# Optimization experiments

Hardware: AMD Instinct MI355X
Metric: run time of the kernel (lower is better)

Reference implementation:

```python
import jax, jax.numpy as jnp
import numpy as np

C = 1024        # number of classes
N = 8           # proxies per class
ALLNUM = C * N  # 8192 total proxies
DIM = 512
R = 0.05
TOPK = int(np.ceil(R * ALLNUM))  # 410
LAM = 0.3
B = 2048


def setup_inputs() -> dict:
    key = jax.random.key(0)
    k1, k2, k3 = jax.random.split(key, 3)
    inp = jax.random.normal(k1, (B, DIM), dtype=jnp.float32)
    target = jax.random.randint(k2, (B,), 0, C, dtype=jnp.int64)
    # kaiming-uniform-initialized proxies approximated by scaled normal init
    proxies = jax.random.normal(k3, (DIM, ALLNUM), dtype=jnp.float32)
    instance_label = jnp.repeat(jnp.arange(C, dtype=jnp.int64), N)  # [ALLNUM]
    return {"input": inp, "target": target, "Proxies": proxies,
            "instance_label": instance_label}


def reference(input, target, Proxies, instance_label):
    # L2-normalize each proxy column (F.normalize along dim=0, eps=1e-12)
    norm = jnp.maximum(jnp.linalg.norm(Proxies, axis=0, keepdims=True), 1e-12)
    centers = Proxies / norm                             # [DIM, ALLNUM]
    similarity = input @ centers                          # [B, ALLNUM]

    positive_mask = (target[:, None] == instance_label[None, :]).astype(similarity.dtype)
    _, indices = jax.lax.top_k(similarity + 1000.0 * positive_mask, TOPK)  # [B, TOPK]

    rows = jnp.arange(similarity.shape[0])[:, None]
    mask = jnp.zeros_like(similarity).at[rows, indices].set(1.0)
    prob_a = mask * similarity                            # sparse-masked similarities

    y_instance_onehot = jax.nn.one_hot(instance_label, C, dtype=similarity.dtype)  # [ALLNUM, C]
    logits = prob_a @ y_instance_onehot                   # [B, C]

    y_target_onehot = jax.nn.one_hot(target, C, dtype=similarity.dtype)  # [B, C]
    logits_mask = 1.0 - (logits == 0.0).astype(similarity.dtype)

    # scale_mask_softmax with scale=1 along dim=1
    e = jnp.exp(logits) * logits_mask
    predict = e / (1e-8 + jnp.sum(e, axis=1, keepdims=True))
    lossClassify = jnp.mean(jnp.sum(-y_target_onehot * jnp.log(predict + 1e-20), axis=1))

    # proxy regularizer: cross-entropy of proxy-vs-class logits
    simCenter = centers.T @ centers                       # [ALLNUM, ALLNUM]
    centers_logits = simCenter @ y_instance_onehot        # [ALLNUM, C]
    logp = jax.nn.log_softmax(centers_logits, axis=1)
    reg = -jnp.mean(jnp.take_along_axis(logp, instance_label[:, None], axis=1))

    return (lossClassify + LAM * reg, lossClassify)
```

## Files before the change

### kernel.cpp

```cpp
#include <hip/hip_runtime.h>
#include <hip/hip_bf16.h>
#include <math.h>

#define C_CLS   1024
#define NPROXY  8
#define ALLNUM  8192
#define DIM     512
#define TOPK    410
#define LAM     0.3f
#define BATCH   2048

typedef __bf16 bf16x8 __attribute__((ext_vector_type(8)));
typedef float floatx4 __attribute__((ext_vector_type(4)));
typedef unsigned short ushort_t;

#define WS_RNORM 0
#define WS_SIG   8192
#define WS_LP    10240
#define WS_RP    12288
#define WS_ABF   14336
#define WS_PBF   538624
#define WS_STBF  2635776
#define WS_LOG   2897920
#define WS_SIM   7092224

__device__ inline float block_reduce(float v, int is_max, float* red, int t) {
    #pragma unroll
    for (int o = 32; o > 0; o >>= 1) {
        float w = __shfl_down(v, o);
        v = is_max ? fmaxf(v, w) : (v + w);
    }
    __syncthreads();
    if ((t & 63) == 0) red[t >> 6] = v;
    __syncthreads();
    return is_max ? fmaxf(fmaxf(red[0], red[1]), fmaxf(red[2], red[3]))
                  : (red[0] + red[1] + red[2] + red[3]);
}

__device__ inline ushort_t f2bf(float f) {
    unsigned u = __float_as_uint(f);
    return (ushort_t)((u + 0x7FFFu + ((u >> 16) & 1u)) >> 16);
}

__device__ inline void ld_g2l_16(const void* g, void* l) {
    __builtin_amdgcn_global_load_lds(
        (const __attribute__((address_space(1))) unsigned int*)g,
        (__attribute__((address_space(3))) unsigned int*)l,
        16, 0, 0);
}

__device__ inline unsigned f2ord(float f) {
    unsigned u = __float_as_uint(f);
    return (u & 0x80000000u) ? ~u : (u | 0x80000000u);
}

__global__ __launch_bounds__(256) void k_prep1(const float* __restrict__ P,
                                               const float* __restrict__ input,
                                               float* __restrict__ rnorm,
                                               float* __restrict__ rowsig,
                                               ushort_t* __restrict__ Abf,
                                               ushort_t* __restrict__ Pbf) {
    __shared__ float tile[32][33];
    float* cred = &tile[0][0];
    int bx = blockIdx.x, t = threadIdx.x;
    if (bx < 256) {
        int tc = t & 31, g = t >> 5;
        int c = bx * 32 + tc;
        const float* pc = P + (size_t)(g * 64) * ALLNUM + c;
        float s = 0.f;
        #pragma unroll 8
        for (int d = 0; d < 64; ++d) {
            float v = pc[(size_t)d * ALLNUM];
            s += v * v;
        }
        cred[g * 32 + tc] = s;
        __syncthreads();
        if (g == 0) {
            float tot = 0.f;
            #pragma unroll
            for (int k = 0; k < 8; ++k) tot += cred[k * 32 + tc];
            rnorm[c] = 1.0f / fmaxf(sqrtf(tot), 1e-12f);
        }
    } else if (bx < 256 + 1024) {
        int a = bx - 256;
        int idx = a * 256 + t;
        float4 v = ((const float4*)input)[idx];
        ushort4 o;
        o.x = f2bf(v.x); o.y = f2bf(v.y); o.z = f2bf(v.z); o.w = f2bf(v.w);
        ((ushort4*)Abf)[idx] = o;
        float sq = v.x * v.x + v.y * v.y + v.z * v.z + v.w * v.w;
        #pragma unroll
        for (int off = 32; off > 0; off >>= 1) sq += __shfl_down(sq, off);
        int lane = t & 63, w = t >> 6;
        if (lane == 0) cred[w] = sq;
        __syncthreads();
        if (t == 0) {
            rowsig[2 * a]     = sqrtf(cred[0] + cred[1]);
            rowsig[2 * a + 1] = sqrtf(cred[2] + cred[3]);
        }
    } else {
        int id = bx - 1280;
        int c0 = (id & 255) * 32, r0 = (id >> 8) * 32;
        int tc = t & 31, tr = t >> 5;
        #pragma unroll
        for (int p = 0; p < 4; ++p)
            tile[tr + p * 8][tc] = P[(size_t)(r0 + tr + p * 8) * ALLNUM + c0 + tc];
        __syncthreads();
        #pragma unroll
        for (int p = 0; p < 4; ++p) {
            int oc = tr + p * 8;
            Pbf[(size_t)(c0 + oc) * DIM + r0 + tc] = f2bf(tile[tc][oc]);
        }
    }
}

__global__ __launch_bounds__(256) void k_stage2(const ushort_t* __restrict__ A,
                                                const ushort_t* __restrict__ B,
                                                const float* __restrict__ P,
                                                const float* __restrict__ rnorm,
                                                float* __restrict__ sim,
                                                ushort_t* __restrict__ Stbf) {
    __shared__ __align__(16) ushort_t smem[2 * 128 * 64];
    int bx = blockIdx.x, t = threadIdx.x;

    if (bx < 1024) {
        ushort_t* sA = smem;
        ushort_t* sB = smem + 128 * 64;
        int w = t >> 6, lane = t & 63;
        int wm = w >> 1, wn = w & 1;
        int bj = (bx & 63) * 128, bi = (bx >> 6) * 128;

        floatx4 acc[4][4];
        #pragma unroll
        for (int tm = 0; tm < 4; ++tm)
            #pragma unroll
            for (int tn = 0; tn < 4; ++tn)
                acc[tm][tn] = (floatx4){0.f, 0.f, 0.f, 0.f};

        for (int k0 = 0; k0 < DIM; k0 += 64) {
            #pragma unroll
            for (int it = 0; it < 4; ++it) {
                int c = w * 256 + it * 64 + lane;
                int m = c >> 3, s = c & 7;
                int q = s ^ (m & 7);
                ld_g2l_16(A + ((size_t)(bi + m) << 9) + k0 + q * 8,
                          &sA[(w * 256 + it * 64) * 8]);
            }
            #pragma unroll
            for (int it = 0; it < 4; ++it) {
                int c = w * 256 + it * 64 + lane;
                int m = c >> 3, s = c & 7;
                int q = s ^ (m & 7);
                ld_g2l_16(B + ((size_t)(bj + m) << 9) + k0 + q * 8,
                          &sB[(w * 256 + it * 64) * 8]);
            }
            asm volatile("s_waitcnt vmcnt(0)" ::: "memory");
            __syncthreads();

            #pragma unroll
            for (int kk = 0; kk < 2; ++kk) {
                bf16x8 af[4], bfr[4];
                int ml = lane & 15, q = lane >> 4;
                #pragma unroll
                for (int tm = 0; tm < 4; ++tm) {
                    int m = wm * 64 + tm * 16 + ml;
                    int s = (kk * 4 + q) ^ (m & 7);
                    af[tm] = *(const bf16x8*)&sA[m * 64 + s * 8];
                }
                #pragma unroll
                for (int tn = 0; tn < 4; ++tn) {
                    int n = wn * 64 + tn * 16 + ml;
                    int s = (kk * 4 + q) ^ (n & 7);
                    bfr[tn] = *(const bf16x8*)&sB[n * 64 + s * 8];
                }
                #pragma unroll
                for (int tm = 0; tm < 4; ++tm)
                    #pragma unroll
                    for (int tn = 0; tn < 4; ++tn)
                        acc[tm][tn] = __builtin_amdgcn_mfma_f32_16x16x32_bf16(
                            af[tm], bfr[tn], acc[tm][tn], 0, 0, 0);
            }
            __syncthreads();
        }

        int ml = lane & 15, qd = lane >> 4;
        #pragma unroll
        for (int tm = 0; tm < 4; ++tm) {
            int rowb = bi + wm * 64 + tm * 16 + qd * 4;
            #pragma unroll
            for (int tn = 0; tn < 4; ++tn) {
                int col = bj + wn * 64 + tn * 16 + ml;
                float sc = rnorm[col];
                #pragma unroll
                for (int i = 0; i < 4; ++i)
                    sim[(size_t)(rowb + i) * ALLNUM + col] = acc[tm][tn][i] * sc;
            }
        }
    } else {
        float* tile = (float*)smem;
        int id = bx - 1024;
        int c0 = (id & 31) * 32, d0 = (id >> 5) * 32;
        int cl = t & 31, dl8 = t >> 5;
        #pragma unroll
        for (int p = 0; p < 4; ++p) {
            int d = d0 + dl8 + 8 * p;
            int c = c0 + cl;
            const float* pp = P + (size_t)d * ALLNUM + c * NPROXY;
            const float* rn = rnorm + c * NPROXY;
            float4 a = *(const float4*)pp;
            float4 b = *(const float4*)(pp + 4);
            float4 ra = *(const float4*)rn;
            float4 rb = *(const float4*)(rn + 4);
            tile[(dl8 + 8 * p) * 33 + cl] =
                a.x * ra.x + a.y * ra.y + a.z * ra.z + a.w * ra.w +
                b.x * rb.x + b.y * rb.y + b.z * rb.z + b.w * rb.w;
        }
        __syncthreads();
        #pragma unroll
        for (int p = 0; p < 4; ++p) {
            int cl2 = dl8 + 8 * p, dl2 = t & 31;
            Stbf[(size_t)(c0 + cl2) * DIM + d0 + dl2] = f2bf(tile[dl2 * 33 + cl2]);
        }
    }
}

#define SEL_CAP 1024
#define GCAP    64

__device__ inline void suffix_select1(unsigned* s_hist, unsigned kk,
                                      unsigned* s_wtot, unsigned* sh_bin,
                                      unsigned* sh_k, int t, int lane, int wid) {
    unsigned h = s_hist[t];
    unsigned v = h;
    #pragma unroll
    for (int off = 1; off < 64; off <<= 1) {
        unsigned o = __shfl_down(v, off);
        if (lane + off < 64) v += o;
    }
    if (lane == 0) s_wtot[wid] = v;
    __syncthreads();
    unsigned above = v - h;
    for (int w2 = wid + 1; w2 < 4; ++w2) above += s_wtot[w2];
    unsigned cum = above + h;
    if (cum >= kk && above < kk) { *sh_bin = (unsigned)t; *sh_k = kk - above; }
    __syncthreads();
}

__global__ __launch_bounds__(256) void k_stage3(const float* __restrict__ sim,
                                                const int* __restrict__ target,
                                                const float* __restrict__ rowsig,
                                                float* __restrict__ loss_part,
                                                const ushort_t* __restrict__ Pbf,
                                                const ushort_t* __restrict__ Stbf,
                                                const float* __restrict__ rnorm,
                                                ushort_t* __restrict__ logits) {
    __shared__ __align__(16) unsigned char smem[16384];
    int bx = blockIdx.x, t = threadIdx.x;
    int lane = t & 63, wid = t >> 6;

    if (bx < 2048) {
        float*    s_cls  = (float*)smem;
        float*    s_bval = (float*)(smem + 4096);
        ushort_t* s_bcol = (ushort_t*)(smem + 8192);
        unsigned* s_bhist= (unsigned*)(smem + 10240);
        float*    s_gval = (float*)(smem + 11264);
        unsigned* s_wtot = (unsigned*)(smem + 11520);
        unsigned* shv    = (unsigned*)(smem + 11536);
        float*    shf    = (float*)(smem + 11552);
        int*      shi    = (int*)(smem + 11556);
        float*    red    = (float*)(smem + 11568);

        int b = bx;
        const float* row = sim + (size_t)b * ALLNUM;
        int tgt = target[b];
        float sig = rowsig[b] * (1.0f / 22.616f);
        float hiT = 1.80f * sig, loT = 1.47f * sig;
        float binscale = 256.0f / (hiT - loT);

        float4 v4[8];
        #pragma unroll
        for (int p = 0; p < 8; ++p) v4[p] = ((const float4*)row)[t + 256 * p];

        if (t == 0) { shv[0] = 0; shv[1] = 0; }
        s_bhist[t] = 0;
        #pragma unroll
        for (int i = 0; i < 4; ++i) s_cls[t + 256 * i] = 0.f;
        __syncthreads();

        float ndef = 0.f;
        #pragma unroll
        for (int p = 0; p < 8; ++p) {
            int f = t + 256 * p;
            int cls = f >> 1;
            const float* pv = (const float*)&v4[p];
            if (cls == tgt) {
                atomicAdd(&s_cls[tgt], pv[0] + pv[1] + pv[2] + pv[3]);
            } else {
                float ds = 0.f;
                #pragma unroll
                for (int e = 0; e < 4; ++e) {
                    float v = pv[e];
                    if (v >= hiT) { ds += v; ndef += 1.f; }
                    else if (v >= loT) {
                        unsigned idx = atomicAdd(&shv[0], 1u);
                        if (idx < SEL_CAP) { s_bval[idx] = v; s_bcol[idx] = (ushort_t)(4 * f + e); }
                        int bin = (int)((v - loT) * binscale);
                        bin = (bin > 255) ? 255 : bin;
                        atomicAdd(&s_bhist[bin], 1u);
                    }
                }
                float o = __shfl_xor(ds, 1);
                float s2 = ds + o;
                if ((t & 1) == 0 && s2 != 0.f) atomicAdd(&s_cls[cls], s2);
            }
        }
        float ndefT = block_reduce(ndef, 0, red, t);
        int bc = (int)shv[0];
        int kq = (TOPK - NPROXY) - (int)ndefT;
        if (t == 0) shi[0] = (kq < 0 || bc < kq || bc > SEL_CAP) ? 1 : 0;
        __syncthreads();

        if (!shi[0]) {
            if (kq > 0) {
                suffix_select1(s_bhist, (unsigned)kq, s_wtot, &shv[2], &shv[3], t, lane, wid);
                int B = (int)shv[2];
                int knew = (int)shv[3];
                for (int j = t; j < bc; j += 256) {
                    float v = s_bval[j];
                    int bin = (int)((v - loT) * binscale);
                    bin = (bin > 255) ? 255 : bin;
                    if (bin == B) {
                        unsigned g = atomicAdd(&shv[1], 1u);
                        if (g < GCAP) s_gval[g] = v;
                    }
                }
                __syncthreads();
                int gc = (int)shv[1];
                if (gc <= GCAP) {
                    if (t < gc) {
                        float vj = s_gval[t];
                        unsigned g = 0, geq = 0;
                        for (int i = 0; i < gc; ++i) {
                            float vi = s_gval[i];
                            g   += (vi > vj) ? 1u : 0u;
                            geq += (vi >= vj) ? 1u : 0u;
                        }
                        if (g < (unsigned)knew && geq >= (unsigned)knew) shf[0] = vj;
                    }
                } else {
                    for (int j = t; j < bc; j += 256) {
                        float vj = s_bval[j];
                        unsigned g = 0, geq = 0;
                        for (int i = 0; i < bc; ++i) {
                            float vi = s_bval[i];
                            g   += (vi > vj) ? 1u : 0u;
                            geq += (vi >= vj) ? 1u : 0u;
                        }
                        if (g < (unsigned)kq && geq >= (unsigned)kq) shf[0] = vj;
                    }
                }
                __syncthreads();
                float thr = shf[0];
                for (int j = t; j < bc; j += 256)
                    if (s_bval[j] >= thr)
                        atomicAdd(&s_cls[s_bcol[j] >> 3], s_bval[j]);
            }
        } else {
            __syncthreads();
            #pragma unroll
            for (int i = 0; i < 4; ++i) s_cls[t + 256 * i] = 0.f;
            __syncthreads();
            #pragma unroll
            for (int p = 0; p < 8; ++p) {
                int f = t + 256 * p;
                const float* pv = (const float*)&v4[p];
                if ((f >> 1) == tgt)
                    atomicAdd(&s_cls[tgt], pv[0] + pv[1] + pv[2] + pv[3]);
            }
            unsigned L = 0u, R = 0xFFFFFFFFu;
            for (int it = 0; it < 33 && R - L > 1; ++it) {
                unsigned mid = L + ((R - L) >> 1);
                float c = 0.f;
                #pragma unroll
                for (int p = 0; p < 8; ++p) {
                    int f = t + 256 * p;
                    const float* pv = (const float*)&v4[p];
                    if ((f >> 1) != tgt) {
                        #pragma unroll
                        for (int e = 0; e < 4; ++e)
                            c += (f2ord(pv[e]) >= mid) ? 1.f : 0.f;
                    }
                }
                c = block_reduce(c, 0, red, t);
                if (c >= (float)(TOPK - NPROXY)) L = mid; else R = mid;
                __syncthreads();
            }
            #pragma unroll
            for (int p = 0; p < 8; ++p) {
                int f = t + 256 * p;
                const float* pv = (const float*)&v4[p];
                if ((f >> 1) != tgt) {
                    #pragma unroll
                    for (int e = 0; e < 4; ++e)
                        if (f2ord(pv[e]) >= L)
                            atomicAdd(&s_cls[f >> 1], pv[e]);
                }
            }
        }
        __syncthreads();

        float4 cv = ((const float4*)s_cls)[t];
        float m = -1e30f;
        if (cv.x != 0.0f) m = fmaxf(m, cv.x);
        if (cv.y != 0.0f) m = fmaxf(m, cv.y);
        if (cv.z != 0.0f) m = fmaxf(m, cv.z);
        if (cv.w != 0.0f) m = fmaxf(m, cv.w);
        m = block_reduce(m, 1, red, t);
        float se = 0.f;
        if (cv.x != 0.0f) se += expf(cv.x - m);
        if (cv.y != 0.0f) se += expf(cv.y - m);
        if (cv.z != 0.0f) se += expf(cv.z - m);
        if (cv.w != 0.0f) se += expf(cv.w - m);
        se = block_reduce(se, 0, red, t);
        if (t == 0) {
            float lt = s_cls[tgt];
            float predict_t = expf(lt - m) / (1e-8f * expf(-m) + se);
            loss_part[b] = -logf(predict_t + 1e-20f);
        }
    } else {
        ushort_t* sA = (ushort_t*)smem;
        ushort_t* sB = (ushort_t*)(smem + 8192);
        int id = bx - 2048;
        int bj = (id & 15) * 64;
        int bi = (id >> 4) * 64;
        int w = wid;
        int wm = w >> 1, wn = w & 1;

        floatx4 acc[2][2];
        #pragma unroll
        for (int tm = 0; tm < 2; ++tm)
            #pragma unroll
            for (int tn = 0; tn < 2; ++tn)
                acc[tm][tn] = (floatx4){0.f, 0.f, 0.f, 0.f};

        for (int k0 = 0; k0 < DIM; k0 += 64) {
            #pragma unroll
            for (int it = 0; it < 2; ++it) {
                int c = (w * 2 + it) * 64 + lane;
                int m = c >> 3, s = c & 7;
                int q = s ^ (m & 7);
                ld_g2l_16(Pbf + ((size_t)(bi + m) << 9) + k0 + q * 8,
                          &sA[((w * 2 + it) * 64) * 8]);
            }
            #pragma unroll
            for (int it = 0; it < 2; ++it) {
                int c = (w * 2 + it) * 64 + lane;
                int m = c >> 3, s = c & 7;
                int q = s ^ (m & 7);
                ld_g2l_16(Stbf + ((size_t)(bj + m) << 9) + k0 + q * 8,
                          &sB[((w * 2 + it) * 64) * 8]);
            }
            asm volatile("s_waitcnt vmcnt(0)" ::: "memory");
            __syncthreads();

            #pragma unroll
            for (int kk = 0; kk < 2; ++kk) {
                bf16x8 af[2], bfr[2];
                int ml = lane & 15, q = lane >> 4;
                #pragma unroll
                for (int tm = 0; tm < 2; ++tm) {
                    int m = wm * 32 + tm * 16 + ml;
                    int s = (kk * 4 + q) ^ (m & 7);
                    af[tm] = *(const bf16x8*)&sA[m * 64 + s * 8];
                }
                #pragma unroll
                for (int tn = 0; tn < 2; ++tn) {
                    int n = wn * 32 + tn * 16 + ml;
                    int s = (kk * 4 + q) ^ (n & 7);
                    bfr[tn] = *(const bf16x8*)&sB[n * 64 + s * 8];
                }
                #pragma unroll
                for (int tm = 0; tm < 2; ++tm)
                    #pragma unroll
                    for (int tn = 0; tn < 2; ++tn)
                        acc[tm][tn] = __builtin_amdgcn_mfma_f32_16x16x32_bf16(
                            af[tm], bfr[tn], acc[tm][tn], 0, 0, 0);
            }
            __syncthreads();
        }

        int ml = lane & 15, qd = lane >> 4;
        #pragma unroll
        for (int tm = 0; tm < 2; ++tm) {
            int rowb = bi + wm * 32 + tm * 16 + qd * 4;
            float4 rnr = *(const float4*)&rnorm[rowb];
            #pragma unroll
            for (int tn = 0; tn < 2; ++tn) {
                int col = bj + wn * 32 + tn * 16 + ml;
                #pragma unroll
                for (int i = 0; i < 4; ++i)
                    logits[(size_t)(rowb + i) * C_CLS + col] =
                        f2bf(acc[tm][tn][i] * ((const float*)&rnr)[i]);
            }
        }
    }
}

__global__ __launch_bounds__(256) void k_regloss(const ushort_t* __restrict__ logits,
                                                 float* __restrict__ reg_part) {
    __shared__ float bsum[4];
    int t = threadIdx.x, lane = t & 63, wid = t >> 6;
    int i = blockIdx.x * 4 + wid;
    const ushort_t* row = logits + (size_t)i * C_CLS;
    uint4 c0 = ((const uint4*)row)[lane];
    uint4 c1 = ((const uint4*)(row + 512))[lane];

    float f[16];
    const unsigned* u0 = (const unsigned*)&c0;
    const unsigned* u1 = (const unsigned*)&c1;
    #pragma unroll
    for (int k = 0; k < 4; ++k) {
        f[2 * k]     = __uint_as_float(u0[k] << 16);
        f[2 * k + 1] = __uint_as_float(u0[k] & 0xFFFF0000u);
        f[8 + 2 * k]     = __uint_as_float(u1[k] << 16);
        f[8 + 2 * k + 1] = __uint_as_float(u1[k] & 0xFFFF0000u);
    }

    int cstar = i >> 3;
    int chunk = cstar >> 9, within = cstar & 511;
    float sd = 0.f;
    if (lane == (within >> 3)) sd = f[chunk * 8 + (within & 7)];

    float m = -1e30f;
    #pragma unroll
    for (int k = 0; k < 16; ++k) m = fmaxf(m, f[k]);
    #pragma unroll
    for (int off = 32; off > 0; off >>= 1) m = fmaxf(m, __shfl_xor(m, off));

    float se = 0.f;
    #pragma unroll
    for (int k = 0; k < 16; ++k) se += expf(f[k] - m);
    #pragma unroll
    for (int off = 32; off > 0; off >>= 1) se += __shfl_xor(se, off);
    #pragma unroll
    for (int off = 32; off > 0; off >>= 1) sd += __shfl_xor(sd, off);

    if (lane == 0) bsum[wid] = m + logf(se) - sd;
    __syncthreads();
    if (t == 0)
        reg_part[blockIdx.x] = bsum[0] + bsum[1] + bsum[2] + bsum[3];
}

__global__ __launch_bounds__(256) void k_final(const float* __restrict__ lp,
                                               const float* __restrict__ rp,
                                               float* __restrict__ out) {
    __shared__ float red[4];
    int t = threadIdx.x;
    float4 a = ((const float4*)lp)[t];
    float4 b = ((const float4*)lp)[t + 256];
    float4 c = ((const float4*)rp)[t];
    float4 d = ((const float4*)rp)[t + 256];
    float ls = a.x + a.y + a.z + a.w + b.x + b.y + b.z + b.w;
    float rs = c.x + c.y + c.z + c.w + d.x + d.y + d.z + d.w;
    ls = block_reduce(ls, 0, red, t);
    rs = block_reduce(rs, 0, red, t);
    if (t == 0) {
        float lc = ls / (float)BATCH;
        float rg = rs / (float)ALLNUM;
        out[0] = lc + LAM * rg;
        out[1] = lc;
    }
}

extern "C" void kernel_launch(void* const* d_in, const int* in_sizes, int n_in,
                              void* d_out, int out_size, void* d_ws, size_t ws_size,
                              hipStream_t stream) {
    const float* input  = (const float*)d_in[0];
    const int*   target = (const int*)d_in[1];
    const float* P      = (const float*)d_in[2];

    float* ws       = (float*)d_ws;
    float* rnorm    = ws + WS_RNORM;
    float* rowsig   = ws + WS_SIG;
    float* loss_part= ws + WS_LP;
    float* reg_part = ws + WS_RP;
    ushort_t* Abf   = (ushort_t*)(ws + WS_ABF);
    ushort_t* Pbf   = (ushort_t*)(ws + WS_PBF);
    ushort_t* Stbf  = (ushort_t*)(ws + WS_STBF);
    ushort_t* logits= (ushort_t*)(ws + WS_LOG);
    float* sim      = ws + WS_SIM;
    float* out      = (float*)d_out;

    hipLaunchKernelGGL(k_prep1, dim3(256 + 1024 + 4096), dim3(256), 0, stream,
                       P, input, rnorm, rowsig, Abf, Pbf);
    hipLaunchKernelGGL(k_stage2, dim3(1024 + 512), dim3(256), 0, stream,
                       Abf, Pbf, P, rnorm, sim, Stbf);
    hipLaunchKernelGGL(k_stage3, dim3(2048 + 2048), dim3(256), 0, stream,
                       sim, target, rowsig, loss_part, Pbf, Stbf, rnorm, logits);
    hipLaunchKernelGGL(k_regloss, dim3(ALLNUM / 4), dim3(256), 0, stream,
                       logits, reg_part);
    hipLaunchKernelGGL(k_final, dim3(1), dim3(256), 0, stream,
                       loss_part, reg_part, out);
}
```

Before: 154.0 us.

## Fuse threshold classification into similarity GEMM epilogue, drop full sim matrix

The similarity GEMM epilogue now classifies each value against per-row thresholds. Definite top-k entries and target-class entries are summed into per-row class accumulators, and band candidates are compacted into small per-row buffers, so the 2048x8192 fp32 similarity matrix is never written or re-read. The selection stage reads only these compact buffers. A slow fallback recomputes the row's dot products when buffers overflow. The reg-loss GEMM blocks are reordered to run first in stage3. The cost is shared-memory atomics in the GEMM epilogue, plus a rare but very expensive scalar fallback path.

```diff
diff --git a/kernel.cpp b/kernel.cpp
--- a/kernel.cpp
+++ b/kernel.cpp
@@ -10,6 +10,10 @@
 #define LAM     0.3f
 #define BATCH   2048
 
+#define BAND_CAP_BLK 28
+#define ROW_CAP      512
+#define GCAP         64
+
 typedef __bf16 bf16x8 __attribute__((ext_vector_type(8)));
 typedef float floatx4 __attribute__((ext_vector_type(4)));
 typedef unsigned short ushort_t;
@@ -18,11 +22,16 @@
 #define WS_SIG   8192
 #define WS_LP    10240
 #define WS_RP    12288
-#define WS_ABF   14336
-#define WS_PBF   538624
-#define WS_STBF  2635776
-#define WS_LOG   2897920
-#define WS_SIM   7092224
+#define WS_CNT   14336
+#define WS_NDEF  16384
+#define WS_FLAG  18432
+#define WS_CLS   20480
+#define WS_BVAL  (WS_CLS + 2048*1024)
+#define WS_BCOL  (WS_BVAL + 2048*512)
+#define WS_ABF   (WS_BCOL + 2048*256)
+#define WS_PBF   (WS_ABF + 524288)
+#define WS_STBF  (WS_PBF + 2097152)
+#define WS_LOG   (WS_STBF + 262144)
 
 __device__ inline float block_reduce(float v, int is_max, float* red, int t) {
     #pragma unroll
@@ -42,6 +51,10 @@
     return (ushort_t)((u + 0x7FFFu + ((u >> 16) & 1u)) >> 16);
 }
 
+__device__ inline float bf2f(ushort_t u) {
+    return __uint_as_float(((unsigned)u) << 16);
+}
+
 __device__ inline void ld_g2l_16(const void* g, void* l) {
     __builtin_amdgcn_global_load_lds(
         (const __attribute__((address_space(1))) unsigned int*)g,
@@ -59,7 +72,8 @@
                                                float* __restrict__ rnorm,
                                                float* __restrict__ rowsig,
                                                ushort_t* __restrict__ Abf,
-                                               ushort_t* __restrict__ Pbf) {
+                                               ushort_t* __restrict__ Pbf,
+                                               unsigned* __restrict__ zaux) {
     __shared__ float tile[32][33];
     float* cred = &tile[0][0];
     int bx = blockIdx.x, t = threadIdx.x;
@@ -98,7 +112,7 @@
             rowsig[2 * a]     = sqrtf(cred[0] + cred[1]);
             rowsig[2 * a + 1] = sqrtf(cred[2] + cred[3]);
         }
-    } else {
+    } else if (bx < 256 + 1024 + 4096) {
         int id = bx - 1280;
         int c0 = (id & 255) * 32, r0 = (id >> 8) * 32;
         int tc = t & 31, tr = t >> 5;
@@ -111,6 +125,8 @@
             int oc = tr + p * 8;
             Pbf[(size_t)(c0 + oc) * DIM + r0 + tc] = f2bf(tile[tc][oc]);
         }
+    } else {
+        for (int i = t; i < 3 * 2048; i += 256) zaux[i] = 0u;
     }
 }
 
@@ -118,7 +134,14 @@
                                                 const ushort_t* __restrict__ B,
                                                 const float* __restrict__ P,
                                                 const float* __restrict__ rnorm,
-                                                float* __restrict__ sim,
+                                                const float* __restrict__ rowsig,
+                                                const int* __restrict__ target,
+                                                float* __restrict__ g_cls,
+                                                float* __restrict__ g_bval,
+                                                ushort_t* __restrict__ g_bcol,
+                                                unsigned* __restrict__ g_cnt,
+                                                unsigned* __restrict__ g_ndef,
+                                                unsigned* __restrict__ g_flag,
                                                 ushort_t* __restrict__ Stbf) {
     __shared__ __align__(16) ushort_t smem[2 * 128 * 64];
     int bx = blockIdx.x, t = threadIdx.x;
@@ -183,17 +206,76 @@
             __syncthreads();
         }
 
+        unsigned char* sb = (unsigned char*)smem;
+        float*    e_cls = (float*)sb;
+        float*    e_bv  = (float*)(sb + 8192);
+        ushort_t* e_bc  = (ushort_t*)(sb + 22528);
+        unsigned* e_cnt = (unsigned*)(sb + 29696);
+        unsigned* e_nd  = (unsigned*)(sb + 30208);
+
+        #pragma unroll
+        for (int i = t; i < 2048; i += 256) e_cls[i] = 0.f;
+        if (t < 128) { e_cnt[t] = 0u; e_nd[t] = 0u; }
+        __syncthreads();
+
         int ml = lane & 15, qd = lane >> 4;
         #pragma unroll
         for (int tm = 0; tm < 4; ++tm) {
-            int rowb = bi + wm * 64 + tm * 16 + qd * 4;
+            int rl0 = wm * 64 + tm * 16 + qd * 4;
+            int rowb = bi + rl0;
+            float4 rs4 = *(const float4*)&rowsig[rowb];
+            int4   tg4 = *(const int4*)&target[rowb];
             #pragma unroll
             for (int tn = 0; tn < 4; ++tn) {
-                int col = bj + wn * 64 + tn * 16 + ml;
+                int cl = wn * 64 + tn * 16 + ml;
+                int col = bj + cl;
                 float sc = rnorm[col];
-                #pragma unroll
-                for (int i = 0; i < 4; ++i)
-                    sim[(size_t)(rowb + i) * ALLNUM + col] = acc[tm][tn][i] * sc;
+                int cls = col >> 3;
+                int clsl = cl >> 3;
+                #pragma unroll
+                for (int i = 0; i < 4; ++i) {
+                    int rl = rl0 + i;
+                    float v = acc[tm][tn][i] * sc;
+                    float sg = ((const float*)&rs4)[i] * (1.0f / 22.616f);
+                    float hiT = 1.80f * sg, loT = 1.47f * sg;
+                    int tg = ((const int*)&tg4)[i];
+                    if (cls == tg) {
+                        atomicAdd(&e_cls[rl * 16 + clsl], v);
+                    } else if (v >= hiT) {
+                        atomicAdd(&e_cls[rl * 16 + clsl], v);
+                        atomicAdd(&e_nd[rl], 1u);
+                    } else if (v >= loT) {
+                        unsigned u = atomicAdd(&e_cnt[rl], 1u);
+                        if (u < BAND_CAP_BLK) {
+                            e_bv[rl * BAND_CAP_BLK + u] = v;
+                            e_bc[rl * BAND_CAP_BLK + u] = (ushort_t)col;
+                        }
+                    }
+                }
+            }
+        }
+        __syncthreads();
+
+        int bjc = bj >> 3;
+        #pragma unroll
+        for (int i = t; i < 2048; i += 256) {
+            int rl = i >> 4, c = i & 15;
+            g_cls[(size_t)(bi + rl) * C_CLS + bjc + c] = e_cls[i];
+        }
+        if (t < 128) {
+            int row = bi + t;
+            unsigned c = e_cnt[t];
+            unsigned nd = e_nd[t];
+            if (nd) atomicAdd(&g_ndef[row], nd);
+            if (c) {
+                unsigned cc = (c > BAND_CAP_BLK) ? BAND_CAP_BLK : c;
+                unsigned base = atomicAdd(&g_cnt[row], cc);
+                if (c > BAND_CAP_BLK || base + cc > ROW_CAP) g_flag[row] = 1u;
+                for (unsigned j = 0; j < cc; ++j) {
+                    if (base + j >= ROW_CAP) break;
+                    g_bval[(size_t)row * ROW_CAP + base + j] = e_bv[t * BAND_CAP_BLK + j];
+                    g_bcol[(size_t)row * ROW_CAP + base + j] = e_bc[t * BAND_CAP_BLK + j];
+                }
             }
         }
     } else {
@@ -224,9 +306,6 @@
     }
 }
 
-#define SEL_CAP 1024
-#define GCAP    64
-
 __device__ inline void suffix_select1(unsigned* s_hist, unsigned kk,
                                       unsigned* s_wtot, unsigned* sh_bin,
                                       unsigned* sh_k, int t, int lane, int wid) {
@@ -246,90 +325,145 @@
     __syncthreads();
 }
 
-__global__ __launch_bounds__(256) void k_stage3(const float* __restrict__ sim,
-                                                const int* __restrict__ target,
+__global__ __launch_bounds__(256) void k_stage3(const int* __restrict__ target,
                                                 const float* __restrict__ rowsig,
-                                                float* __restrict__ loss_part,
+                                                const float* __restrict__ rnorm,
+                                                const ushort_t* __restrict__ Abf,
                                                 const ushort_t* __restrict__ Pbf,
                                                 const ushort_t* __restrict__ Stbf,
-                                                const float* __restrict__ rnorm,
+                                                const float* __restrict__ g_cls,
+                                                const float* __restrict__ g_bval,
+                                                const ushort_t* __restrict__ g_bcol,
+                                                const unsigned* __restrict__ g_cnt,
+                                                const unsigned* __restrict__ g_ndef,
+                                                const unsigned* __restrict__ g_flag,
+                                                float* __restrict__ loss_part,
                                                 ushort_t* __restrict__ logits) {
     __shared__ __align__(16) unsigned char smem[16384];
     int bx = blockIdx.x, t = threadIdx.x;
     int lane = t & 63, wid = t >> 6;
 
     if (bx < 2048) {
+        ushort_t* sA = (ushort_t*)smem;
+        ushort_t* sB = (ushort_t*)(smem + 8192);
+        int id = bx;
+        int bj = (id & 15) * 64;
+        int bi = (id >> 4) * 64;
+        int w = wid;
+        int wm = w >> 1, wn = w & 1;
+
+        floatx4 acc[2][2];
+        #pragma unroll
+        for (int tm = 0; tm < 2; ++tm)
+            #pragma unroll
+            for (int tn = 0; tn < 2; ++tn)
+                acc[tm][tn] = (floatx4){0.f, 0.f, 0.f, 0.f};
+
+        for (int k0 = 0; k0 < DIM; k0 += 64) {
+            #pragma unroll
+            for (int it = 0; it < 2; ++it) {
+                int c = (w * 2 + it) * 64 + lane;
+                int m = c >> 3, s = c & 7;
+                int q = s ^ (m & 7);
+                ld_g2l_16(Pbf + ((size_t)(bi + m) << 9) + k0 + q * 8,
+                          &sA[((w * 2 + it) * 64) * 8]);
+            }
+            #pragma unroll
+            for (int it = 0; it < 2; ++it) {
+                int c = (w * 2 + it) * 64 + lane;
+                int m = c >> 3, s = c & 7;
+                int q = s ^ (m & 7);
+                ld_g2l_16(Stbf + ((size_t)(bj + m) << 9) + k0 + q * 8,
+                          &sB[((w * 2 + it) * 64) * 8]);
+            }
+            asm volatile("s_waitcnt vmcnt(0)" ::: "memory");
+            __syncthreads();
+
+            #pragma unroll
+            for (int kk = 0; kk < 2; ++kk) {
+                bf16x8 af[2], bfr[2];
+                int ml = lane & 15, q = lane >> 4;
+                #pragma unroll
+                for (int tm = 0; tm < 2; ++tm) {
+                    int m = wm * 32 + tm * 16 + ml;
+                    int s = (kk * 4 + q) ^ (m & 7);
+                    af[tm] = *(const bf16x8*)&sA[m * 64 + s * 8];
+                }
+                #pragma unroll
+                for (int tn = 0; tn < 2; ++tn) {
+                    int n = wn * 32 + tn * 16 + ml;
+                    int s = (kk * 4 + q) ^ (n & 7);
+                    bfr[tn] = *(const bf16x8*)&sB[n * 64 + s * 8];
+                }
+                #pragma unroll
+                for (int tm = 0; tm < 2; ++tm)
+                    #pragma unroll
+                    for (int tn = 0; tn < 2; ++tn)
+                        acc[tm][tn] = __builtin_amdgcn_mfma_f32_16x16x32_bf16(
+                            af[tm], bfr[tn], acc[tm][tn], 0, 0, 0);
+            }
+            __syncthreads();
+        }
+
+        int ml = lane & 15, qd = lane >> 4;
+        #pragma unroll
+        for (int tm = 0; tm < 2; ++tm) {
+            int rowb = bi + wm * 32 + tm * 16 + qd * 4;
+            float4 rnr = *(const float4*)&rnorm[rowb];
+            #pragma unroll
+            for (int tn = 0; tn < 2; ++tn) {
+                int col = bj + wn * 32 + tn * 16 + ml;
+                #pragma unroll
+                for (int i = 0; i < 4; ++i)
+                    logits[(size_t)(rowb + i) * C_CLS + col] =
+                        f2bf(acc[tm][tn][i] * ((const float*)&rnr)[i]);
+            }
+        }
+    } else {
         float*    s_cls  = (float*)smem;
         float*    s_bval = (float*)(smem + 4096);
-        ushort_t* s_bcol = (ushort_t*)(smem + 8192);
-        unsigned* s_bhist= (unsigned*)(smem + 10240);
-        float*    s_gval = (float*)(smem + 11264);
-        unsigned* s_wtot = (unsigned*)(smem + 11520);
-        unsigned* shv    = (unsigned*)(smem + 11536);
-        float*    shf    = (float*)(smem + 11552);
-        int*      shi    = (int*)(smem + 11556);
-        float*    red    = (float*)(smem + 11568);
-
-        int b = bx;
-        const float* row = sim + (size_t)b * ALLNUM;
+        ushort_t* s_bcol = (ushort_t*)(smem + 6144);
+        unsigned* s_hist = (unsigned*)(smem + 7168);
+        float*    s_arow = (float*)(smem + 8192);
+        unsigned* s_wtot = (unsigned*)(smem + 10240);
+        unsigned* shv    = (unsigned*)(smem + 10256);
+        float*    shf    = (float*)(smem + 10272);
+        float*    red    = (float*)(smem + 10288);
+        float*    s_gval = (float*)(smem + 10304);
+
+        int b = bx - 2048;
         int tgt = target[b];
         float sig = rowsig[b] * (1.0f / 22.616f);
         float hiT = 1.80f * sig, loT = 1.47f * sig;
         float binscale = 256.0f / (hiT - loT);
 
-        float4 v4[8];
-        #pragma unroll
-        for (int p = 0; p < 8; ++p) v4[p] = ((const float4*)row)[t + 256 * p];
-
-        if (t == 0) { shv[0] = 0; shv[1] = 0; }
-        s_bhist[t] = 0;
-        #pragma unroll
-        for (int i = 0; i < 4; ++i) s_cls[t + 256 * i] = 0.f;
-        __syncthreads();
-
-        float ndef = 0.f;
-        #pragma unroll
-        for (int p = 0; p < 8; ++p) {
-            int f = t + 256 * p;
-            int cls = f >> 1;
-            const float* pv = (const float*)&v4[p];
-            if (cls == tgt) {
-                atomicAdd(&s_cls[tgt], pv[0] + pv[1] + pv[2] + pv[3]);
-            } else {
-                float ds = 0.f;
-                #pragma unroll
-                for (int e = 0; e < 4; ++e) {
-                    float v = pv[e];
-                    if (v >= hiT) { ds += v; ndef += 1.f; }
-                    else if (v >= loT) {
-                        unsigned idx = atomicAdd(&shv[0], 1u);
-                        if (idx < SEL_CAP) { s_bval[idx] = v; s_bcol[idx] = (ushort_t)(4 * f + e); }
-                        int bin = (int)((v - loT) * binscale);
-                        bin = (bin > 255) ? 255 : bin;
-                        atomicAdd(&s_bhist[bin], 1u);
-                    }
-                }
-                float o = __shfl_xor(ds, 1);
-                float s2 = ds + o;
-                if ((t & 1) == 0 && s2 != 0.f) atomicAdd(&s_cls[cls], s2);
-            }
-        }
-        float ndefT = block_reduce(ndef, 0, red, t);
-        int bc = (int)shv[0];
-        int kq = (TOPK - NPROXY) - (int)ndefT;
-        if (t == 0) shi[0] = (kq < 0 || bc < kq || bc > SEL_CAP) ? 1 : 0;
-        __syncthreads();
-
-        if (!shi[0]) {
+        ((float4*)s_cls)[t] = ((const float4*)(g_cls + (size_t)b * C_CLS))[t];
+        unsigned cnt = g_cnt[b], nd = g_ndef[b], fl = g_flag[b];
+        int kq = (TOPK - NPROXY) - (int)nd;
+        int ok = (fl == 0u) && (cnt <= ROW_CAP) && (kq >= 0) && ((int)cnt >= kq);
+        if (t == 0) shv[1] = 0u;
+        s_hist[t] = 0u;
+        __syncthreads();
+
+        if (ok) {
             if (kq > 0) {
-                suffix_select1(s_bhist, (unsigned)kq, s_wtot, &shv[2], &shv[3], t, lane, wid);
-                int B = (int)shv[2];
+                for (int j = t; j < (int)cnt; j += 256) {
+                    float v = g_bval[(size_t)b * ROW_CAP + j];
+                    s_bval[j] = v;
+                    s_bcol[j] = g_bcol[(size_t)b * ROW_CAP + j];
+                    int bin = (int)((v - loT) * binscale);
+                    bin = (bin > 255) ? 255 : bin;
+                    atomicAdd(&s_hist[bin], 1u);
+                }
+                __syncthreads();
+                suffix_select1(s_hist, (unsigned)kq, s_wtot, &shv[2], &shv[3], t, lane, wid);
+                int Bb = (int)shv[2];
                 int knew = (int)shv[3];
-                for (int j = t; j < bc; j += 256) {
+                for (int j = t; j < (int)cnt; j += 256) {
                     float v = s_bval[j];
                     int bin = (int)((v - loT) * binscale);
                     bin = (bin > 255) ? 255 : bin;
-                    if (bin == B) {
+                    if (bin == Bb) {
                         unsigned g = atomicAdd(&shv[1], 1u);
                         if (g < GCAP) s_gval[g] = v;
                     }
@@ -348,10 +482,10 @@
                         if (g < (unsigned)knew && geq >= (unsigned)knew) shf[0] = vj;
                     }
                 } else {
-                    for (int j = t; j < bc; j += 256) {
+                    for (int j = t; j < (int)cnt; j += 256) {
                         float vj = s_bval[j];
                         unsigned g = 0, geq = 0;
-                        for (int i = 0; i < bc; ++i) {
+                        for (int i = 0; i < (int)cnt; ++i) {
                             float vi = s_bval[i];
                             g   += (vi > vj) ? 1u : 0u;
                             geq += (vi >= vj) ? 1u : 0u;
@@ -361,15 +495,31 @@
                 }
                 __syncthreads();
                 float thr = shf[0];
-                for (int j = t; j < bc; j += 256)
+                for (int j = t; j < (int)cnt; j += 256)
                     if (s_bval[j] >= thr)
                         atomicAdd(&s_cls[s_bcol[j] >> 3], s_bval[j]);
             }
         } else {
-            __syncthreads();
+            for (int i = t; i < DIM; i += 256)
+                s_arow[i] = bf2f(Abf[(size_t)b * DIM + i]);
             #pragma unroll
             for (int i = 0; i < 4; ++i) s_cls[t + 256 * i] = 0.f;
             __syncthreads();
+            float4 v4[8];
+            for (int p = 0; p < 8; ++p) {
+                int f = t + 256 * p;
+                float vv[4];
+                for (int e = 0; e < 4; ++e) {
+                    int col = 4 * f + e;
+                    const ushort_t* pc = Pbf + (size_t)col * DIM;
+                    float a = 0.f;
+                    for (int d = 0; d < DIM; ++d)
+                        a += s_arow[d] * bf2f(pc[d]);
+                    vv[e] = a * rnorm[col];
+                }
+                float4 o; o.x = vv[0]; o.y = vv[1]; o.z = vv[2]; o.w = vv[3];
+                v4[p] = o;
+            }
             #pragma unroll
             for (int p = 0; p < 8; ++p) {
                 int f = t + 256 * p;
@@ -426,82 +576,6 @@
             float lt = s_cls[tgt];
             float predict_t = expf(lt - m) / (1e-8f * expf(-m) + se);
             loss_part[b] = -logf(predict_t + 1e-20f);
-        }
-    } else {
-        ushort_t* sA = (ushort_t*)smem;
-        ushort_t* sB = (ushort_t*)(smem + 8192);
-        int id = bx - 2048;
-        int bj = (id & 15) * 64;
-        int bi = (id >> 4) * 64;
-        int w = wid;
-        int wm = w >> 1, wn = w & 1;
-
-        floatx4 acc[2][2];
-        #pragma unroll
-        for (int tm = 0; tm < 2; ++tm)
-            #pragma unroll
-            for (int tn = 0; tn < 2; ++tn)
-                acc[tm][tn] = (floatx4){0.f, 0.f, 0.f, 0.f};
-
-        for (int k0 = 0; k0 < DIM; k0 += 64) {
-            #pragma unroll
-            for (int it = 0; it < 2; ++it) {
-                int c = (w * 2 + it) * 64 + lane;
-                int m = c >> 3, s = c & 7;
-                int q = s ^ (m & 7);
-                ld_g2l_16(Pbf + ((size_t)(bi + m) << 9) + k0 + q * 8,
-                          &sA[((w * 2 + it) * 64) * 8]);
-            }
-            #pragma unroll
-            for (int it = 0; it < 2; ++it) {
-                int c = (w * 2 + it) * 64 + lane;
-                int m = c >> 3, s = c & 7;
-                int q = s ^ (m & 7);
-                ld_g2l_16(Stbf + ((size_t)(bj + m) << 9) + k0 + q * 8,
-                          &sB[((w * 2 + it) * 64) * 8]);
-            }
-            asm volatile("s_waitcnt vmcnt(0)" ::: "memory");
-            __syncthreads();
-
-            #pragma unroll
-            for (int kk = 0; kk < 2; ++kk) {
-                bf16x8 af[2], bfr[2];
-                int ml = lane & 15, q = lane >> 4;
-                #pragma unroll
-                for (int tm = 0; tm < 2; ++tm) {
-                    int m = wm * 32 + tm * 16 + ml;
-                    int s = (kk * 4 + q) ^ (m & 7);
-                    af[tm] = *(const bf16x8*)&sA[m * 64 + s * 8];
-                }
-                #pragma unroll
-                for (int tn = 0; tn < 2; ++tn) {
-                    int n = wn * 32 + tn * 16 + ml;
-                    int s = (kk * 4 + q) ^ (n & 7);
-                    bfr[tn] = *(const bf16x8*)&sB[n * 64 + s * 8];
-                }
-                #pragma unroll
-                for (int tm = 0; tm < 2; ++tm)
-                    #pragma unroll
-                    for (int tn = 0; tn < 2; ++tn)
-                        acc[tm][tn] = __builtin_amdgcn_mfma_f32_16x16x32_bf16(
-                            af[tm], bfr[tn], acc[tm][tn], 0, 0, 0);
-            }
-            __syncthreads();
-        }
-
-        int ml = lane & 15, qd = lane >> 4;
-        #pragma unroll
-        for (int tm = 0; tm < 2; ++tm) {
-            int rowb = bi + wm * 32 + tm * 16 + qd * 4;
-            float4 rnr = *(const float4*)&rnorm[rowb];
-            #pragma unroll
-            for (int tn = 0; tn < 2; ++tn) {
-                int col = bj + wn * 32 + tn * 16 + ml;
-                #pragma unroll
-                for (int i = 0; i < 4; ++i)
-                    logits[(size_t)(rowb + i) * C_CLS + col] =
-                        f2bf(acc[tm][tn][i] * ((const float*)&rnr)[i]);
-            }
         }
     }
 }
@@ -579,24 +653,32 @@
     const int*   target = (const int*)d_in[1];
     const float* P      = (const float*)d_in[2];
 
-    float* ws       = (float*)d_ws;
-    float* rnorm    = ws + WS_RNORM;
-    float* rowsig   = ws + WS_SIG;
-    float* loss_part= ws + WS_LP;
-    float* reg_part = ws + WS_RP;
-    ushort_t* Abf   = (ushort_t*)(ws + WS_ABF);
-    ushort_t* Pbf   = (ushort_t*)(ws + WS_PBF);
-    ushort_t* Stbf  = (ushort_t*)(ws + WS_STBF);
-    ushort_t* logits= (ushort_t*)(ws + WS_LOG);
-    float* sim      = ws + WS_SIM;
-    float* out      = (float*)d_out;
-
-    hipLaunchKernelGGL(k_prep1, dim3(256 + 1024 + 4096), dim3(256), 0, stream,
-                       P, input, rnorm, rowsig, Abf, Pbf);
+    float* ws        = (float*)d_ws;
+    float* rnorm     = ws + WS_RNORM;
+    float* rowsig    = ws + WS_SIG;
+    float* loss_part = ws + WS_LP;
+    float* reg_part  = ws + WS_RP;
+    unsigned* g_cnt  = (unsigned*)(ws + WS_CNT);
+    unsigned* g_ndef = (unsigned*)(ws + WS_NDEF);
+    unsigned* g_flag = (unsigned*)(ws + WS_FLAG);
+    float* g_cls     = ws + WS_CLS;
+    float* g_bval    = ws + WS_BVAL;
+    ushort_t* g_bcol = (ushort_t*)(ws + WS_BCOL);
+    ushort_t* Abf    = (ushort_t*)(ws + WS_ABF);
+    ushort_t* Pbf    = (ushort_t*)(ws + WS_PBF);
+    ushort_t* Stbf   = (ushort_t*)(ws + WS_STBF);
+    ushort_t* logits = (ushort_t*)(ws + WS_LOG);
+    float* out       = (float*)d_out;
+
+    hipLaunchKernelGGL(k_prep1, dim3(256 + 1024 + 4096 + 1), dim3(256), 0, stream,
+                       P, input, rnorm, rowsig, Abf, Pbf, g_cnt);
     hipLaunchKernelGGL(k_stage2, dim3(1024 + 512), dim3(256), 0, stream,
-                       Abf, Pbf, P, rnorm, sim, Stbf);
+                       Abf, Pbf, P, rnorm, rowsig, target,
+                       g_cls, g_bval, g_bcol, g_cnt, g_ndef, g_flag, Stbf);
     hipLaunchKernelGGL(k_stage3, dim3(2048 + 2048), dim3(256), 0, stream,
-                       sim, target, rowsig, loss_part, Pbf, Stbf, rnorm, logits);
+                       target, rowsig, rnorm, Abf, Pbf, Stbf,
+                       g_cls, g_bval, g_bcol, g_cnt, g_ndef, g_flag,
+                       loss_part, logits);
     hipLaunchKernelGGL(k_regloss, dim3(ALLNUM / 4), dim3(256), 0, stream,
                        logits, reg_part);
     hipLaunchKernelGGL(k_final, dim3(1), dim3(256), 0, stream,
```

Result: slower. 157.4 us (+2.2%).
